# Optimization experiments

Hardware: AMD Instinct MI355X
Metric: run time of the kernel (lower is better)

Reference implementation:

```python
import jax, jax.numpy as jnp
import numpy as np

NUM_CLASSES = 100
NUM_PROTOS = 10
FEAT_DIM = 1024
BATCH = 16384
NALL = NUM_CLASSES * NUM_PROTOS


def setup_inputs() -> dict:
    key = jax.random.key(0)
    k1, k2, k3 = jax.random.split(key, 3)
    x = jax.random.normal(k1, (BATCH, FEAT_DIM), dtype=jnp.float32)
    protos = jax.random.normal(k2, (NALL, FEAT_DIM), dtype=jnp.float32)
    enc_w = jax.random.normal(k3, (FEAT_DIM, FEAT_DIM), dtype=jnp.float32) / np.sqrt(FEAT_DIM)
    enc_b = jnp.zeros((FEAT_DIM,), dtype=jnp.float32)
    return {"x": x, "protos": protos, "enc_w": enc_w, "enc_b": enc_b}


def reference(x, protos, enc_w, enc_b):
    # encoder(protos): linear projection, (nall, F)
    ep = protos @ enc_w + enc_b
    # Pairwise euclidean distance via GEMM-based squared-distance trick:
    x_sq = jnp.sum(x * x, axis=-1, keepdims=True)            # (B, 1)
    p_sq = jnp.sum(ep * ep, axis=-1)                          # (nall,)
    d2 = x_sq - 2.0 * (x @ ep.T) + p_sq[None, :]              # (B, nall)
    d = jnp.sqrt(jnp.maximum(d2, 0.0))                        # L2 norm, clamp fp error
    # reshape matches torch: index = proto * num_classes + class
    d = d.reshape(x.shape[0], NUM_PROTOS, NUM_CLASSES)
    return jnp.min(d, axis=1)                                 # (B, num_classes)
```

## Files before the change

kernel.cpp:

```cpp
#include <hip/hip_runtime.h>
#include <hip/hip_bf16.h>
#include <stdint.h>

#define FEAT 1024
#define NALL 1000
#define NCLS 100

typedef __attribute__((ext_vector_type(8))) short short8;
typedef __attribute__((ext_vector_type(4))) float f32x4;
typedef __attribute__((ext_vector_type(4))) unsigned short us4;

__device__ __forceinline__ unsigned short f2bf(float f) {
    union { float f; uint32_t u; } v; v.f = f;
    uint32_t u = v.u;
    return (unsigned short)((u + 0x7FFFu + ((u >> 16) & 1u)) >> 16);
}

__device__ __forceinline__ void gload16(const void* g, void* l) {
    __builtin_amdgcn_global_load_lds((__attribute__((address_space(1))) void*)g,
                                     (__attribute__((address_space(3))) void*)l,
                                     16, 0, 0);
}

__global__ __launch_bounds__(256) void k_prep_x(const float* __restrict__ x,
                                                unsigned short* __restrict__ xb,
                                                float* __restrict__ xsq) {
    int row = blockIdx.x * 4 + (threadIdx.x >> 6);
    int lane = threadIdx.x & 63;
    const float4* xr = (const float4*)(x + (size_t)row * FEAT);
    float s = 0.f;
#pragma unroll
    for (int i = 0; i < 4; ++i) {
        float4 v = xr[lane + i * 64];
        s += v.x * v.x + v.y * v.y + v.z * v.z + v.w * v.w;
        us4 o;
        o[0] = f2bf(v.x); o[1] = f2bf(v.y); o[2] = f2bf(v.z); o[3] = f2bf(v.w);
        *(us4*)(xb + (size_t)row * FEAT + (size_t)(lane + i * 64) * 4) = o;
    }
#pragma unroll
    for (int off = 32; off; off >>= 1) s += __shfl_xor(s, off);
    if (lane == 0) xsq[row] = s;
}

__global__ __launch_bounds__(256) void k_prep_protos(const float* __restrict__ p,
                                                     unsigned short* __restrict__ pb) {
    int row = blockIdx.x;
    int t = threadIdx.x;
    us4 o;
    if (row < NALL) {
        float4 v = ((const float4*)(p + (size_t)row * FEAT))[t];
        o[0] = f2bf(v.x); o[1] = f2bf(v.y); o[2] = f2bf(v.z); o[3] = f2bf(v.w);
    } else {
        o[0] = 0; o[1] = 0; o[2] = 0; o[3] = 0;
    }
    *(us4*)(pb + (size_t)row * FEAT + (size_t)t * 4) = o;
}

__global__ __launch_bounds__(256) void k_transpose_w(const float* __restrict__ w,
                                                     unsigned short* __restrict__ wt) {
    __shared__ float tile[32][33];
    int bx = blockIdx.x, by = blockIdx.y;
    int tx = threadIdx.x & 31, ty = threadIdx.x >> 5;
#pragma unroll
    for (int i = 0; i < 4; ++i) {
        int r = by * 32 + ty + i * 8;
        tile[ty + i * 8][tx] = w[(size_t)r * FEAT + bx * 32 + tx];
    }
    __syncthreads();
#pragma unroll
    for (int i = 0; i < 4; ++i) {
        int r = bx * 32 + ty + i * 8;
        wt[(size_t)r * FEAT + by * 32 + tx] = f2bf(tile[tx][ty + i * 8]);
    }
}

__global__ __launch_bounds__(256) void k_enc_gemm(const unsigned short* __restrict__ A,
                                                  const unsigned short* __restrict__ B,
                                                  const float* __restrict__ bias,
                                                  unsigned short* __restrict__ epb) {
    __shared__ __align__(16) char smem[32768];
    int bm0 = (blockIdx.x >> 3) * 128;
    int bn0 = (blockIdx.x & 7) * 128;
    int tid = threadIdx.x, lane = tid & 63, wid = tid >> 6;
    int wm = wid >> 1, wn = wid & 1;
    int ls = lane >> 4, lf = lane & 15;
    f32x4 acc[4][4] = {};
    for (int k0 = 0; k0 < FEAT; k0 += 64) {
        __syncthreads();
#pragma unroll
        for (int i = 0; i < 4; ++i) {
            int ci = wid + i * 4;
            int r = ci * 8 + (lane >> 3), c = (lane & 7) * 8;
            gload16(A + (size_t)(bm0 + r) * FEAT + k0 + c, smem + ci * 1024);
            gload16(B + (size_t)(bn0 + r) * FEAT + k0 + c, smem + 16384 + ci * 1024);
        }
        __syncthreads();
#pragma unroll
        for (int kk = 0; kk < 64; kk += 32) {
            short8 a[4], b[4];
#pragma unroll
            for (int f = 0; f < 4; ++f) {
                a[f] = *(const short8*)(smem + (wm * 64 + f * 16 + lf) * 128 + (kk + ls * 8) * 2);
                b[f] = *(const short8*)(smem + 16384 + (wn * 64 + f * 16 + lf) * 128 + (kk + ls * 8) * 2);
            }
#pragma unroll
            for (int fm = 0; fm < 4; ++fm)
#pragma unroll
                for (int fn = 0; fn < 4; ++fn)
                    acc[fm][fn] = __builtin_amdgcn_mfma_f32_16x16x32_bf16(a[fm], b[fn], acc[fm][fn], 0, 0, 0);
        }
    }
    int tr = ls * 4, tc = lf;
#pragma unroll
    for (int fn = 0; fn < 4; ++fn) {
        int col = bn0 + wn * 64 + fn * 16 + tc;
        float bb = bias[col];
#pragma unroll
        for (int fm = 0; fm < 4; ++fm) {
#pragma unroll
            for (int r = 0; r < 4; ++r) {
                int row = bm0 + wm * 64 + fm * 16 + tr + r;
                if (row < NALL) {
                    int pr = (row % 100) * 10 + row / 100;
                    epb[(size_t)pr * FEAT + col] = f2bf(acc[fm][fn][r] + bb);
                }
            }
        }
    }
}

__global__ __launch_bounds__(256) void k_psq(const unsigned short* __restrict__ epb,
                                             float* __restrict__ psq) {
    int row = blockIdx.x * 4 + (threadIdx.x >> 6);
    int lane = threadIdx.x & 63;
    if (row >= NALL) return;
    float s = 0.f;
    const short8* r8 = (const short8*)(epb + (size_t)row * FEAT);
#pragma unroll
    for (int i = 0; i < 2; ++i) {
        short8 v = r8[lane + i * 64];
#pragma unroll
        for (int j = 0; j < 8; ++j) {
            union { uint32_t u; float f; } c;
            c.u = ((uint32_t)(unsigned short)v[j]) << 16;
            s += c.f * c.f;
        }
    }
#pragma unroll
    for (int off = 32; off; off >>= 1) s += __shfl_xor(s, off);
    if (lane == 0) psq[row] = s;
}

__global__ __launch_bounds__(256, 4) void k_main(const unsigned short* __restrict__ xb,
                                                 const unsigned short* __restrict__ epb,
                                                 const float* __restrict__ xsq,
                                                 const float* __restrict__ psq,
                                                 float* __restrict__ out) {
    __shared__ __align__(16) char smem[27648];
    const int bid = blockIdx.x;
    const int swz = (bid & 7) * 208 + (bid >> 3);
    const int bm0 = (swz / 13) * 128;
    const int nt  = swz % 13;
    const int bn0 = (nt < 12) ? nt * 80 : 920;
    const int cls0 = (nt < 12) ? nt * 8 : 92;
    const int tid = threadIdx.x, lane = tid & 63, wid = tid >> 6;
    const int ls = lane >> 4, lf = lane & 15;
    float* xsq_s = (float*)(smem + 26624);
    float* psq_s = (float*)(smem + 27136);
    if (tid < 128) xsq_s[tid] = xsq[bm0 + tid];
    if (tid < 80)  psq_s[tid] = psq[bn0 + tid];

    const int sr = lane >> 3, scb = lane & 7;
    const int scol = ((scb ^ sr) << 3);
    const unsigned short* aptr[4];
    const unsigned short* bptr[3];
#pragma unroll
    for (int i = 0; i < 4; ++i)
        aptr[i] = xb + (size_t)(bm0 + (wid + i * 4) * 8 + sr) * FEAT + scol;
#pragma unroll
    for (int j = 0; j < 3; ++j) {
        int cj = wid + j * 4;
        bptr[j] = epb + (size_t)(bn0 + (cj < 10 ? cj : 0) * 8 + sr) * FEAT + scol;
    }

    int raA[2], raB[5];
#pragma unroll
    for (int f = 0; f < 2; ++f) raA[f] = (wid * 32 + f * 16 + lf) * 128;
#pragma unroll
    for (int f = 0; f < 5; ++f) raB[f] = 16384 + (f * 16 + lf) * 128;
    const int sw = lf & 7;

    f32x4 acc[2][5] = {};

    for (int t = 0; t < 16; ++t) {
        __syncthreads();
#pragma unroll
        for (int i = 0; i < 4; ++i)
            gload16(aptr[i], smem + (wid + i * 4) * 1024);
#pragma unroll
        for (int j = 0; j < 3; ++j) {
            int cj = wid + j * 4;
            if (cj < 10) gload16(bptr[j], smem + 16384 + cj * 1024);
        }
#pragma unroll
        for (int i = 0; i < 4; ++i) aptr[i] += 64;
#pragma unroll
        for (int j = 0; j < 3; ++j) bptr[j] += 64;
        __syncthreads();
#pragma unroll
        for (int kk2 = 0; kk2 < 2; ++kk2) {
            const int off = (((kk2 * 4 + ls) ^ sw) << 4);
            short8 a[2], b[5];
#pragma unroll
            for (int f = 0; f < 2; ++f)
                a[f] = *(const short8*)(smem + raA[f] + off);
#pragma unroll
            for (int f = 0; f < 5; ++f)
                b[f] = *(const short8*)(smem + raB[f] + off);
#pragma unroll
            for (int fm = 0; fm < 2; ++fm)
#pragma unroll
                for (int fn = 0; fn < 5; ++fn)
                    acc[fm][fn] = __builtin_amdgcn_mfma_f32_16x16x32_bf16(a[fm], b[fn], acc[fm][fn], 0, 0, 0);
        }
    }

    float* dls = (float*)smem;
    const int tr = ls * 4;
#pragma unroll
    for (int p = 0; p < 2; ++p) {
        __syncthreads();
#pragma unroll
        for (int fn = 0; fn < 5; ++fn) {
            int col = fn * 16 + lf;
            float pq = psq_s[col];
#pragma unroll
            for (int r = 0; r < 4; ++r) {
                float d2 = xsq_s[wid * 32 + p * 16 + tr + r] - 2.f * acc[p][fn][r] + pq;
                dls[(wid * 16 + tr + r) * 81 + col] = sqrtf(fmaxf(d2, 0.f));
            }
        }
        __syncthreads();
#pragma unroll
        for (int i = 0; i < 2; ++i) {
            int task = tid + i * 256;
            int rr = task >> 3, cl = task & 7;
            float m = 1e30f;
#pragma unroll
            for (int j = 0; j < 10; ++j) m = fminf(m, dls[rr * 81 + cl * 10 + j]);
            int grow = bm0 + (rr >> 4) * 32 + p * 16 + (rr & 15);
            out[(size_t)grow * NCLS + cls0 + cl] = m;
        }
    }
}

extern "C" void kernel_launch(void* const* d_in, const int* in_sizes, int n_in,
                              void* d_out, int out_size, void* d_ws, size_t ws_size,
                              hipStream_t stream) {
    const float* x      = (const float*)d_in[0];
    const float* protos = (const float*)d_in[1];
    const float* enc_w  = (const float*)d_in[2];
    const float* enc_b  = (const float*)d_in[3];
    float* out = (float*)d_out;
    char* ws = (char*)d_ws;

    unsigned short* xb  = (unsigned short*)ws;
    unsigned short* epb = (unsigned short*)(ws + 33554432);
    unsigned short* prb = (unsigned short*)(ws + 35651584);
    unsigned short* wtb = (unsigned short*)(ws + 37748736);
    float* xsq = (float*)(ws + 39845888);
    float* psq = (float*)(ws + 39911424);

    k_prep_x<<<4096, 256, 0, stream>>>(x, xb, xsq);
    k_prep_protos<<<1024, 256, 0, stream>>>(protos, prb);
    k_transpose_w<<<dim3(32, 32), 256, 0, stream>>>(enc_w, wtb);
    k_enc_gemm<<<64, 256, 0, stream>>>(prb, wtb, enc_b, epb);
    k_psq<<<250, 256, 0, stream>>>(epb, psq);
    k_main<<<1664, 256, 0, stream>>>(xb, epb, xsq, psq, out);
}
```

Measured before the change: 101.7 us.

## Double-buffer prototype tiles, read x from global directly, fuse prep kernels, shrink encoder tiles

The main distance kernel now loads x fragments straight from global memory into registers instead of staging them through LDS. It double-buffers only the prototype tile in LDS, prefetching the next K slice while computing the current one, so each step needs one barrier instead of two. The proto-cast and weight-transpose kernels are merged into one launch, and the encoder GEMM uses 64x64 tiles over 256 blocks for more parallelism. Direct global A loads are uncoalesced per lane and rely on L2/cache hits, which risks more memory latency.

```diff
diff --git a/kernel.cpp b/kernel.cpp
--- a/kernel.cpp
+++ b/kernel.cpp
@@ -42,35 +42,37 @@
     if (lane == 0) xsq[row] = s;
 }
 
-__global__ __launch_bounds__(256) void k_prep_protos(const float* __restrict__ p,
-                                                     unsigned short* __restrict__ pb) {
-    int row = blockIdx.x;
-    int t = threadIdx.x;
-    us4 o;
-    if (row < NALL) {
-        float4 v = ((const float4*)(p + (size_t)row * FEAT))[t];
-        o[0] = f2bf(v.x); o[1] = f2bf(v.y); o[2] = f2bf(v.z); o[3] = f2bf(v.w);
+__global__ __launch_bounds__(256) void k_prep_pw(const float* __restrict__ p,
+                                                 unsigned short* __restrict__ pb,
+                                                 const float* __restrict__ w,
+                                                 unsigned short* __restrict__ wt) {
+    __shared__ float tile[32][33];
+    int b = blockIdx.x;
+    if (b < 1024) {
+        int row = b, t = threadIdx.x;
+        us4 o;
+        if (row < NALL) {
+            float4 v = ((const float4*)(p + (size_t)row * FEAT))[t];
+            o[0] = f2bf(v.x); o[1] = f2bf(v.y); o[2] = f2bf(v.z); o[3] = f2bf(v.w);
+        } else {
+            o[0] = 0; o[1] = 0; o[2] = 0; o[3] = 0;
+        }
+        *(us4*)(pb + (size_t)row * FEAT + (size_t)t * 4) = o;
     } else {
-        o[0] = 0; o[1] = 0; o[2] = 0; o[3] = 0;
-    }
-    *(us4*)(pb + (size_t)row * FEAT + (size_t)t * 4) = o;
-}
-
-__global__ __launch_bounds__(256) void k_transpose_w(const float* __restrict__ w,
-                                                     unsigned short* __restrict__ wt) {
-    __shared__ float tile[32][33];
-    int bx = blockIdx.x, by = blockIdx.y;
-    int tx = threadIdx.x & 31, ty = threadIdx.x >> 5;
-#pragma unroll
-    for (int i = 0; i < 4; ++i) {
-        int r = by * 32 + ty + i * 8;
-        tile[ty + i * 8][tx] = w[(size_t)r * FEAT + bx * 32 + tx];
-    }
-    __syncthreads();
-#pragma unroll
-    for (int i = 0; i < 4; ++i) {
-        int r = bx * 32 + ty + i * 8;
-        wt[(size_t)r * FEAT + by * 32 + tx] = f2bf(tile[tx][ty + i * 8]);
+        int bb = b - 1024;
+        int bx = bb & 31, by = bb >> 5;
+        int tx = threadIdx.x & 31, ty = threadIdx.x >> 5;
+#pragma unroll
+        for (int i = 0; i < 4; ++i) {
+            int r = by * 32 + ty + i * 8;
+            tile[ty + i * 8][tx] = w[(size_t)r * FEAT + bx * 32 + tx];
+        }
+        __syncthreads();
+#pragma unroll
+        for (int i = 0; i < 4; ++i) {
+            int r = bx * 32 + ty + i * 8;
+            wt[(size_t)r * FEAT + by * 32 + tx] = f2bf(tile[tx][ty + i * 8]);
+        }
     }
 }
 
@@ -78,48 +80,48 @@
                                                   const unsigned short* __restrict__ B,
                                                   const float* __restrict__ bias,
                                                   unsigned short* __restrict__ epb) {
-    __shared__ __align__(16) char smem[32768];
-    int bm0 = (blockIdx.x >> 3) * 128;
-    int bn0 = (blockIdx.x & 7) * 128;
+    __shared__ __align__(16) char smem[16384];
+    int bm0 = (blockIdx.x >> 4) * 64;
+    int bn0 = (blockIdx.x & 15) * 64;
     int tid = threadIdx.x, lane = tid & 63, wid = tid >> 6;
     int wm = wid >> 1, wn = wid & 1;
     int ls = lane >> 4, lf = lane & 15;
-    f32x4 acc[4][4] = {};
+    f32x4 acc[2][2] = {};
     for (int k0 = 0; k0 < FEAT; k0 += 64) {
         __syncthreads();
 #pragma unroll
-        for (int i = 0; i < 4; ++i) {
+        for (int i = 0; i < 2; ++i) {
             int ci = wid + i * 4;
             int r = ci * 8 + (lane >> 3), c = (lane & 7) * 8;
             gload16(A + (size_t)(bm0 + r) * FEAT + k0 + c, smem + ci * 1024);
-            gload16(B + (size_t)(bn0 + r) * FEAT + k0 + c, smem + 16384 + ci * 1024);
+            gload16(B + (size_t)(bn0 + r) * FEAT + k0 + c, smem + 8192 + ci * 1024);
         }
         __syncthreads();
 #pragma unroll
         for (int kk = 0; kk < 64; kk += 32) {
-            short8 a[4], b[4];
-#pragma unroll
-            for (int f = 0; f < 4; ++f) {
-                a[f] = *(const short8*)(smem + (wm * 64 + f * 16 + lf) * 128 + (kk + ls * 8) * 2);
-                b[f] = *(const short8*)(smem + 16384 + (wn * 64 + f * 16 + lf) * 128 + (kk + ls * 8) * 2);
-            }
-#pragma unroll
-            for (int fm = 0; fm < 4; ++fm)
-#pragma unroll
-                for (int fn = 0; fn < 4; ++fn)
+            short8 a[2], b[2];
+#pragma unroll
+            for (int f = 0; f < 2; ++f) {
+                a[f] = *(const short8*)(smem + (wm * 32 + f * 16 + lf) * 128 + (kk + ls * 8) * 2);
+                b[f] = *(const short8*)(smem + 8192 + (wn * 32 + f * 16 + lf) * 128 + (kk + ls * 8) * 2);
+            }
+#pragma unroll
+            for (int fm = 0; fm < 2; ++fm)
+#pragma unroll
+                for (int fn = 0; fn < 2; ++fn)
                     acc[fm][fn] = __builtin_amdgcn_mfma_f32_16x16x32_bf16(a[fm], b[fn], acc[fm][fn], 0, 0, 0);
         }
     }
     int tr = ls * 4, tc = lf;
 #pragma unroll
-    for (int fn = 0; fn < 4; ++fn) {
-        int col = bn0 + wn * 64 + fn * 16 + tc;
+    for (int fn = 0; fn < 2; ++fn) {
+        int col = bn0 + wn * 32 + fn * 16 + tc;
         float bb = bias[col];
 #pragma unroll
-        for (int fm = 0; fm < 4; ++fm) {
+        for (int fm = 0; fm < 2; ++fm) {
 #pragma unroll
             for (int r = 0; r < 4; ++r) {
-                int row = bm0 + wm * 64 + fm * 16 + tr + r;
+                int row = bm0 + wm * 32 + fm * 16 + tr + r;
                 if (row < NALL) {
                     int pr = (row % 100) * 10 + row / 100;
                     epb[(size_t)pr * FEAT + col] = f2bf(acc[fm][fn][r] + bb);
@@ -156,7 +158,7 @@
                                                  const float* __restrict__ xsq,
                                                  const float* __restrict__ psq,
                                                  float* __restrict__ out) {
-    __shared__ __align__(16) char smem[27648];
+    __shared__ __align__(16) char smem[22016];
     const int bid = blockIdx.x;
     const int swz = (bid & 7) * 208 + (bid >> 3);
     const int bm0 = (swz / 13) * 128;
@@ -165,64 +167,70 @@
     const int cls0 = (nt < 12) ? nt * 8 : 92;
     const int tid = threadIdx.x, lane = tid & 63, wid = tid >> 6;
     const int ls = lane >> 4, lf = lane & 15;
-    float* xsq_s = (float*)(smem + 26624);
-    float* psq_s = (float*)(smem + 27136);
+    float* xsq_s = (float*)(smem + 20992);
+    float* psq_s = (float*)(smem + 21504);
     if (tid < 128) xsq_s[tid] = xsq[bm0 + tid];
     if (tid < 80)  psq_s[tid] = psq[bn0 + tid];
 
+    const unsigned short* ga[2];
+#pragma unroll
+    for (int f = 0; f < 2; ++f)
+        ga[f] = xb + (size_t)(bm0 + wid * 32 + f * 16 + lf) * FEAT + ls * 8;
+
     const int sr = lane >> 3, scb = lane & 7;
     const int scol = ((scb ^ sr) << 3);
-    const unsigned short* aptr[4];
     const unsigned short* bptr[3];
-#pragma unroll
-    for (int i = 0; i < 4; ++i)
-        aptr[i] = xb + (size_t)(bm0 + (wid + i * 4) * 8 + sr) * FEAT + scol;
 #pragma unroll
     for (int j = 0; j < 3; ++j) {
         int cj = wid + j * 4;
         bptr[j] = epb + (size_t)(bn0 + (cj < 10 ? cj : 0) * 8 + sr) * FEAT + scol;
     }
 
-    int raA[2], raB[5];
-#pragma unroll
-    for (int f = 0; f < 2; ++f) raA[f] = (wid * 32 + f * 16 + lf) * 128;
-#pragma unroll
-    for (int f = 0; f < 5; ++f) raB[f] = 16384 + (f * 16 + lf) * 128;
+    int raB[5];
+#pragma unroll
+    for (int f = 0; f < 5; ++f) raB[f] = (f * 16 + lf) * 128;
     const int sw = lf & 7;
 
     f32x4 acc[2][5] = {};
 
+#pragma unroll
+    for (int j = 0; j < 3; ++j) {
+        int cj = wid + j * 4;
+        if (cj < 10) gload16(bptr[j], smem + cj * 1024);
+    }
+    __syncthreads();
+
+#pragma unroll
     for (int t = 0; t < 16; ++t) {
-        __syncthreads();
-#pragma unroll
-        for (int i = 0; i < 4; ++i)
-            gload16(aptr[i], smem + (wid + i * 4) * 1024);
-#pragma unroll
-        for (int j = 0; j < 3; ++j) {
-            int cj = wid + j * 4;
-            if (cj < 10) gload16(bptr[j], smem + 16384 + cj * 1024);
-        }
-#pragma unroll
-        for (int i = 0; i < 4; ++i) aptr[i] += 64;
-#pragma unroll
-        for (int j = 0; j < 3; ++j) bptr[j] += 64;
-        __syncthreads();
-#pragma unroll
-        for (int kk2 = 0; kk2 < 2; ++kk2) {
-            const int off = (((kk2 * 4 + ls) ^ sw) << 4);
-            short8 a[2], b[5];
-#pragma unroll
-            for (int f = 0; f < 2; ++f)
-                a[f] = *(const short8*)(smem + raA[f] + off);
+        const char* base = (const char*)smem + (t & 1) * 10240;
+        short8 a[2][2];
+#pragma unroll
+        for (int f = 0; f < 2; ++f)
+#pragma unroll
+            for (int k2 = 0; k2 < 2; ++k2)
+                a[f][k2] = *(const short8*)(ga[f] + t * 64 + k2 * 32);
+        if (t < 15) {
+            char* nb = (char*)smem + ((t + 1) & 1) * 10240;
+#pragma unroll
+            for (int j = 0; j < 3; ++j) {
+                int cj = wid + j * 4;
+                if (cj < 10) gload16(bptr[j] + (t + 1) * 64, nb + cj * 1024);
+            }
+        }
+#pragma unroll
+        for (int k2 = 0; k2 < 2; ++k2) {
+            const int off = (((k2 * 4 + ls) ^ sw) << 4);
+            short8 b[5];
 #pragma unroll
             for (int f = 0; f < 5; ++f)
-                b[f] = *(const short8*)(smem + raB[f] + off);
+                b[f] = *(const short8*)(base + raB[f] + off);
 #pragma unroll
             for (int fm = 0; fm < 2; ++fm)
 #pragma unroll
                 for (int fn = 0; fn < 5; ++fn)
-                    acc[fm][fn] = __builtin_amdgcn_mfma_f32_16x16x32_bf16(a[fm], b[fn], acc[fm][fn], 0, 0, 0);
-        }
+                    acc[fm][fn] = __builtin_amdgcn_mfma_f32_16x16x32_bf16(a[fm][k2], b[fn], acc[fm][fn], 0, 0, 0);
+        }
+        __syncthreads();
     }
 
     float* dls = (float*)smem;
@@ -272,9 +280,8 @@
     float* psq = (float*)(ws + 39911424);
 
     k_prep_x<<<4096, 256, 0, stream>>>(x, xb, xsq);
-    k_prep_protos<<<1024, 256, 0, stream>>>(protos, prb);
-    k_transpose_w<<<dim3(32, 32), 256, 0, stream>>>(enc_w, wtb);
-    k_enc_gemm<<<64, 256, 0, stream>>>(prb, wtb, enc_b, epb);
+    k_prep_pw<<<2048, 256, 0, stream>>>(protos, prb, enc_w, wtb);
+    k_enc_gemm<<<256, 256, 0, stream>>>(prb, wtb, enc_b, epb);
     k_psq<<<250, 256, 0, stream>>>(epb, psq);
     k_main<<<1664, 256, 0, stream>>>(xb, epb, xsq, psq, out);
 }
```

New measurement: 108.1 us. 1.06x slower.
